# Performance work log

Measured on AMD Instinct MI355X. Metric: run time of the kernel, lower is better.

## Reference

```python
import jax, jax.numpy as jnp
import numpy as np

N, E, T = 10000, 50000, 80000   # nodes, edges, triplets
D, H, C, CF = 16, 128, 64, 64   # n_orb, hidden_dim, conv_dim, coeffs_dim


def l2norm(v):
    # matches torch F.normalize(dim=-1): x / max(||x||_2, 1e-12)
    return v / jnp.maximum(jnp.linalg.norm(v, axis=-1, keepdims=True), 1e-12)


def setup_inputs() -> dict:
    key = jax.random.key(0)
    ks = jax.random.split(key, 16)

    def w(k, i, o):
        return jax.random.normal(k, (i, o), jnp.float32) / np.sqrt(i).astype(np.float32)

    return {
        "x": jax.random.normal(ks[0], (N, H), jnp.float32),
        "cji": jax.random.normal(ks[1], (E, D, CF), jnp.float32),
        "robs": jax.random.normal(ks[2], (E, D), jnp.float32),
        "shbs": jax.random.normal(ks[3], (T, D), jnp.float32),
        "idx_i": jax.random.randint(ks[4], (E,), 0, N),
        "idx_j": jax.random.randint(ks[5], (E,), 0, N),
        "tri_idx_k": jax.random.randint(ks[6], (T,), 0, N),
        "edge_idx_kj": jax.random.randint(ks[7], (T,), 0, E),
        "edge_idx_ji": jax.random.randint(ks[8], (T,), 0, E),
        "W_nb": w(ks[9], H, 2 * C), "b_nb": jnp.zeros((2 * C,), jnp.float32),
        "W_c1": w(ks[10], CF, C),
        "W_c2": w(ks[11], C, 2 * C),
        "W_t3": w(ks[12], C, C), "b_t3": jnp.zeros((C,), jnp.float32),
        "W_n1": w(ks[13], 2 * C, C), "b_n1": jnp.zeros((C,), jnp.float32),
        "W_n2": w(ks[14], C, C), "b_n2": jnp.zeros((C,), jnp.float32),
        "W_na": w(ks[15], C, H),
    }


def reference(x, cji, robs, shbs, idx_i, idx_j, tri_idx_k, edge_idx_kj,
              edge_idx_ji, W_nb, b_nb, W_c1, W_c2, W_t3, b_t3, W_n1, b_n1,
              W_n2, b_n2, W_na):
    silu = jax.nn.silu
    # node_before_lin + chunk
    h = x @ W_nb + b_nb                       # [N, 2C]
    xq, xk = jnp.split(h, 2, axis=-1)         # each [N, C]
    # coeffs_before_lin: act -> Dense -> act -> Dense (no biases)
    c = silu(silu(cji) @ W_c1) @ W_c2         # [E, D, 2C]
    cji2, ckj = jnp.split(c, 2, axis=-1)      # each [E, D, C]
    # triplet gathers
    ckj_g = l2norm(ckj[edge_idx_kj])          # [T, D, C]
    tbo = l2norm(jnp.einsum('td,tdh->th', shbs * robs[edge_idx_kj], ckj_g))  # [T, C]
    tbw = tbo * jax.nn.sigmoid(xk[tri_idx_k])  # [T, C]
    # scatter triplets -> edges (dim_size = robs.size(0) = E)
    agg = jax.ops.segment_sum(tbw, edge_idx_ji, num_segments=E)  # [E, C]
    tbw2 = silu(agg) @ W_t3 + b_t3            # three_lin, [E, C]
    cji3 = l2norm(cji2 * (1.0 + tbw2[:, None, :]))  # cji + cji*w, normalized
    lcao = l2norm(jnp.einsum('ed,edh->eh', robs, cji3))  # [E, C]
    # node message: node_lin on concatenated endpoint features
    m = jnp.concatenate([xq[idx_i], xq[idx_j]], axis=-1)  # [E, 2C]
    m = silu(silu(m) @ W_n1 + b_n1) @ W_n2 + b_n2          # [E, C]
    out = x + jax.ops.segment_sum(lcao * m, idx_i, num_segments=N) @ W_na
    return out
```

## Files before the change

### kernel.cpp

```cpp
#include <hip/hip_runtime.h>
#include <hip/hip_bf16.h>

#define NN 10000
#define EE 50000
#define TT 80000
#define DD 16
#define HH 128
#define CC 64

typedef __hip_bfloat16 bf16;
typedef __attribute__((ext_vector_type(8))) short bf16x8;
typedef __attribute__((ext_vector_type(4))) float f32x4;

__device__ __forceinline__ float silu_f(float x) { return x / (1.f + __expf(-x)); }
__device__ __forceinline__ float sigm_f(float x) { return 1.f / (1.f + __expf(-x)); }

__device__ __forceinline__ short f2bs(float x) {
  __hip_bfloat16 h = __float2bfloat16(x);
  short s;
  __builtin_memcpy(&s, &h, 2);
  return s;
}

__device__ __forceinline__ float rnorm_f(float ss) {
  return __builtin_amdgcn_rcpf(fmaxf(__builtin_amdgcn_sqrtf(ss), 1e-12f));
}

__device__ __forceinline__ float wave_sum64(float v) {
#pragma unroll
  for (int m = 1; m < 64; m <<= 1) v += __shfl_xor(v, m, 64);
  return v;
}

__device__ __forceinline__ void bf2x(unsigned u, float& lo, float& hi) {
  lo = __uint_as_float(u << 16);
  hi = __uint_as_float(u & 0xffff0000u);
}

__global__ __launch_bounds__(128) void k_node(
    const float* __restrict__ x, const float* __restrict__ W_nb,
    const float* __restrict__ b_nb, float* __restrict__ sxq,
    float* __restrict__ sigxk) {
  __shared__ float xrow[HH];
  const int n = blockIdx.x;
  const int t = threadIdx.x;
  xrow[t] = x[(size_t)n * HH + t];
  __syncthreads();
  float acc = b_nb[t];
#pragma unroll 8
  for (int k = 0; k < HH; ++k) acc = fmaf(xrow[k], W_nb[k * HH + t], acc);
  if (t < CC)
    sxq[(size_t)n * CC + t] = silu_f(acc);
  else
    sigxk[(size_t)n * CC + (t - CC)] = sigm_f(acc);
}

#define K2_BLOCKS 2048
#define K2_TILES 50000
__global__ __launch_bounds__(256, 2) void k_coeffs(
    const float* __restrict__ cji, const float* __restrict__ W_c1,
    const float* __restrict__ W_c2, bf16* __restrict__ cji2,
    bf16* __restrict__ ckjn) {
  __shared__ __align__(16) short xbuf[4][16 * 72];
  const int tid = threadIdx.x;
  const int w = tid >> 6, l = tid & 63;
  const int lr = l & 15, lg = l >> 4;
  short* mybuf = xbuf[w];

  bf16x8 b1[2][4];
  bf16x8 b2[2][8];
#pragma unroll
  for (int kt = 0; kt < 2; ++kt) {
#pragma unroll
    for (int nt = 0; nt < 4; ++nt) {
      bf16x8 t;
#pragma unroll
      for (int b = 0; b < 8; ++b)
        t[b] = f2bs(W_c1[(kt * 32 + lg * 8 + b) * 64 + nt * 16 + lr]);
      b1[kt][nt] = t;
    }
#pragma unroll
    for (int nt = 0; nt < 8; ++nt) {
      bf16x8 t;
#pragma unroll
      for (int b = 0; b < 8; ++b)
        t[b] = f2bs(W_c2[(kt * 32 + lg * 8 + b) * 128 + nt * 16 + lr]);
      b2[kt][nt] = t;
    }
  }

  const int nwave = K2_BLOCKS * 4;
  int tile = blockIdx.x * 4 + w;
  if (tile >= K2_TILES) return;

  float4 r0, r1, r2, r3;
  {
    const float* Ab = cji + (size_t)tile * 16 * 64 + lr * 64 + lg * 8;
    r0 = *(const float4*)(Ab);
    r1 = *(const float4*)(Ab + 4);
    r2 = *(const float4*)(Ab + 32);
    r3 = *(const float4*)(Ab + 36);
  }

  for (; tile < K2_TILES; tile += nwave) {
    bf16x8 a0, a1;
    a0[0] = f2bs(silu_f(r0.x)); a0[1] = f2bs(silu_f(r0.y));
    a0[2] = f2bs(silu_f(r0.z)); a0[3] = f2bs(silu_f(r0.w));
    a0[4] = f2bs(silu_f(r1.x)); a0[5] = f2bs(silu_f(r1.y));
    a0[6] = f2bs(silu_f(r1.z)); a0[7] = f2bs(silu_f(r1.w));
    a1[0] = f2bs(silu_f(r2.x)); a1[1] = f2bs(silu_f(r2.y));
    a1[2] = f2bs(silu_f(r2.z)); a1[3] = f2bs(silu_f(r2.w));
    a1[4] = f2bs(silu_f(r3.x)); a1[5] = f2bs(silu_f(r3.y));
    a1[6] = f2bs(silu_f(r3.z)); a1[7] = f2bs(silu_f(r3.w));

    const int next = tile + nwave;
    if (next < K2_TILES) {
      const float* Ab = cji + (size_t)next * 16 * 64 + lr * 64 + lg * 8;
      r0 = *(const float4*)(Ab);
      r1 = *(const float4*)(Ab + 4);
      r2 = *(const float4*)(Ab + 32);
      r3 = *(const float4*)(Ab + 36);
    }

    f32x4 acc1[4];
#pragma unroll
    for (int nt = 0; nt < 4; ++nt) acc1[nt] = (f32x4){0.f, 0.f, 0.f, 0.f};
#pragma unroll
    for (int nt = 0; nt < 4; ++nt) {
      acc1[nt] = __builtin_amdgcn_mfma_f32_16x16x32_bf16(a0, b1[0][nt], acc1[nt], 0, 0, 0);
      acc1[nt] = __builtin_amdgcn_mfma_f32_16x16x32_bf16(a1, b1[1][nt], acc1[nt], 0, 0, 0);
    }

#pragma unroll
    for (int nt = 0; nt < 4; ++nt)
#pragma unroll
      for (int j = 0; j < 4; ++j)
        mybuf[(lg * 4 + j) * 72 + nt * 16 + lr] = f2bs(silu_f(acc1[nt][j]));

    bf16x8 a20 = *(const bf16x8*)(mybuf + lr * 72 + lg * 8);
    bf16x8 a21 = *(const bf16x8*)(mybuf + lr * 72 + 32 + lg * 8);

    f32x4 acc2[8];
#pragma unroll
    for (int nt = 0; nt < 8; ++nt) acc2[nt] = (f32x4){0.f, 0.f, 0.f, 0.f};
#pragma unroll
    for (int nt = 0; nt < 8; ++nt) {
      acc2[nt] = __builtin_amdgcn_mfma_f32_16x16x32_bf16(a20, b2[0][nt], acc2[nt], 0, 0, 0);
      acc2[nt] = __builtin_amdgcn_mfma_f32_16x16x32_bf16(a21, b2[1][nt], acc2[nt], 0, 0, 0);
    }

    float rn[4];
#pragma unroll
    for (int j = 0; j < 4; ++j) {
      float ss = acc2[4][j] * acc2[4][j];
      ss = fmaf(acc2[5][j], acc2[5][j], ss);
      ss = fmaf(acc2[6][j], acc2[6][j], ss);
      ss = fmaf(acc2[7][j], acc2[7][j], ss);
#pragma unroll
      for (int m = 1; m < 16; m <<= 1) ss += __shfl_xor(ss, m, 64);
      rn[j] = rnorm_f(ss);
    }

    union { short h[16]; uint4 u[2]; } p;
#pragma unroll
    for (int nt = 0; nt < 4; ++nt)
#pragma unroll
      for (int j = 0; j < 4; ++j) p.h[nt * 4 + j] = f2bs(acc2[nt][j]);
    {
      uint4* d0 = (uint4*)(cji2 + (size_t)tile * 1024 + l * 16);
      d0[0] = p.u[0];
      d0[1] = p.u[1];
    }
#pragma unroll
    for (int nt = 0; nt < 4; ++nt)
#pragma unroll
      for (int j = 0; j < 4; ++j) p.h[nt * 4 + j] = f2bs(acc2[4 + nt][j] * rn[j]);
    {
      uint4* d1 = (uint4*)(ckjn + (size_t)tile * 1024 + l * 16);
      d1[0] = p.u[0];
      d1[1] = p.u[1];
    }
  }
}

__global__ __launch_bounds__(256) void k_triplet(
    const bf16* __restrict__ ckjn, const float* __restrict__ shbs,
    const float* __restrict__ robs, const float* __restrict__ sigxk,
    const int* __restrict__ tri_idx_k, const int* __restrict__ edge_idx_kj,
    const int* __restrict__ edge_idx_ji, float* __restrict__ agg) {
  const int wid = (blockIdx.x * 256 + threadIdx.x) >> 6;
  const int l = threadIdx.x & 63;
  if (wid >= TT) return;
  const int lq = l >> 4, lr = l & 15;
  const int kj = edge_idx_kj[wid];
  const int kn = tri_idx_k[wid];
  const int ji = edge_idx_ji[wid];
  const float4 sh = *(const float4*)(shbs + (size_t)wid * DD + lq * 4);
  const float4 rb = *(const float4*)(robs + (size_t)kj * DD + lq * 4);
  const float w0 = sh.x * rb.x, w1 = sh.y * rb.y, w2 = sh.z * rb.z,
              w3 = sh.w * rb.w;
  const uint4* base = (const uint4*)(ckjn + (size_t)kj * 1024 + l * 16);
  const uint4 u0 = base[0], u1 = base[1];
  float acc[4];
  {
    float x0, x1, x2, x3;
    bf2x(u0.x, x0, x1); bf2x(u0.y, x2, x3);
    acc[0] = fmaf(w3, x3, fmaf(w2, x2, fmaf(w1, x1, w0 * x0)));
    bf2x(u0.z, x0, x1); bf2x(u0.w, x2, x3);
    acc[1] = fmaf(w3, x3, fmaf(w2, x2, fmaf(w1, x1, w0 * x0)));
    bf2x(u1.x, x0, x1); bf2x(u1.y, x2, x3);
    acc[2] = fmaf(w3, x3, fmaf(w2, x2, fmaf(w1, x1, w0 * x0)));
    bf2x(u1.z, x0, x1); bf2x(u1.w, x2, x3);
    acc[3] = fmaf(w3, x3, fmaf(w2, x2, fmaf(w1, x1, w0 * x0)));
  }
#pragma unroll
  for (int m = 16; m < 64; m <<= 1)
#pragma unroll
    for (int q = 0; q < 4; ++q) acc[q] += __shfl_xor(acc[q], m, 64);
  const float sel = (lq == 0) ? acc[0] : (lq == 1) ? acc[1] : (lq == 2) ? acc[2] : acc[3];
  const float ss = wave_sum64(sel * sel);
  const float tbw = sel * rnorm_f(ss) * sigxk[(size_t)kn * CC + l];
  atomicAdd(&agg[(size_t)ji * CC + l], tbw);
}

#define K4A_TILES 3125
__global__ __launch_bounds__(256, 2) void k_edge_a(
    const float* __restrict__ agg, const float* __restrict__ sxq,
    const int* __restrict__ idx_i, const int* __restrict__ idx_j,
    const float* __restrict__ W_t3, const float* __restrict__ b_t3,
    const float* __restrict__ W_n1, const float* __restrict__ b_n1,
    const float* __restrict__ W_n2, const float* __restrict__ b_n2,
    float* __restrict__ onew_buf, float* __restrict__ m_buf) {
  __shared__ __align__(16) float fbuf[4][16 * 68];
  __shared__ __align__(16) short sbuf[4][16 * 72];
  const int tid = threadIdx.x;
  const int w = tid >> 6, l = tid & 63;
  const int lr = l & 15, lg = l >> 4;
  float* fb = fbuf[w];
  short* sb = sbuf[w];
  const int tile = blockIdx.x * 4 + w;
  if (tile >= K4A_TILES) return;

  bf16x8 bt3[2][4], bn1[4][4], bn2[2][4];
#pragma unroll
  for (int kt = 0; kt < 2; ++kt)
#pragma unroll
    for (int nt = 0; nt < 4; ++nt) {
      bf16x8 t;
#pragma unroll
      for (int b = 0; b < 8; ++b)
        t[b] = f2bs(W_t3[(kt * 32 + lg * 8 + b) * 64 + nt * 16 + lr]);
      bt3[kt][nt] = t;
    }
#pragma unroll
  for (int kt = 0; kt < 4; ++kt)
#pragma unroll
    for (int nt = 0; nt < 4; ++nt) {
      bf16x8 t;
#pragma unroll
      for (int b = 0; b < 8; ++b)
        t[b] = f2bs(W_n1[(kt * 32 + lg * 8 + b) * 64 + nt * 16 + lr]);
      bn1[kt][nt] = t;
    }
#pragma unroll
  for (int kt = 0; kt < 2; ++kt)
#pragma unroll
    for (int nt = 0; nt < 4; ++nt) {
      bf16x8 t;
#pragma unroll
      for (int b = 0; b < 8; ++b)
        t[b] = f2bs(W_n2[(kt * 32 + lg * 8 + b) * 64 + nt * 16 + lr]);
      bn2[kt][nt] = t;
    }
  float bt3c[4], bn1c[4], bn2c[4];
#pragma unroll
  for (int nt = 0; nt < 4; ++nt) {
    bt3c[nt] = b_t3[nt * 16 + lr];
    bn1c[nt] = b_n1[nt * 16 + lr];
    bn2c[nt] = b_n2[nt * 16 + lr];
  }

  const int e = tile * 16 + lr;
  const int vi = idx_i[e], vj = idx_j[e];

  bf16x8 aagg[2];
#pragma unroll
  for (int kt = 0; kt < 2; ++kt) {
    const float4 u = *(const float4*)(agg + (size_t)e * 64 + kt * 32 + lg * 8);
    const float4 v = *(const float4*)(agg + (size_t)e * 64 + kt * 32 + lg * 8 + 4);
    bf16x8 t;
    t[0] = f2bs(silu_f(u.x)); t[1] = f2bs(silu_f(u.y));
    t[2] = f2bs(silu_f(u.z)); t[3] = f2bs(silu_f(u.w));
    t[4] = f2bs(silu_f(v.x)); t[5] = f2bs(silu_f(v.y));
    t[6] = f2bs(silu_f(v.z)); t[7] = f2bs(silu_f(v.w));
    aagg[kt] = t;
  }
  f32x4 acc[4];
#pragma unroll
  for (int nt = 0; nt < 4; ++nt) acc[nt] = (f32x4){0.f, 0.f, 0.f, 0.f};
#pragma unroll
  for (int nt = 0; nt < 4; ++nt) {
    acc[nt] = __builtin_amdgcn_mfma_f32_16x16x32_bf16(aagg[0], bt3[0][nt], acc[nt], 0, 0, 0);
    acc[nt] = __builtin_amdgcn_mfma_f32_16x16x32_bf16(aagg[1], bt3[1][nt], acc[nt], 0, 0, 0);
  }
#pragma unroll
  for (int nt = 0; nt < 4; ++nt)
#pragma unroll
    for (int j = 0; j < 4; ++j)
      fb[(lg * 4 + j) * 68 + nt * 16 + lr] = 1.f + bt3c[nt] + acc[nt][j];
  {
    const int row = l >> 2, cs = (l & 3) * 16;
    float* dst = onew_buf + (size_t)(tile * 16 + row) * 64 + cs;
#pragma unroll
    for (int q = 0; q < 4; ++q)
      *(float4*)(dst + q * 4) = *(const float4*)(fb + row * 68 + cs + q * 4);
  }

  bf16x8 am[4];
#pragma unroll
  for (int kt = 0; kt < 4; ++kt) {
    const float* src = (kt < 2) ? (sxq + (size_t)vi * 64 + kt * 32)
                                : (sxq + (size_t)vj * 64 + (kt - 2) * 32);
    const float4 u = *(const float4*)(src + lg * 8);
    const float4 v = *(const float4*)(src + lg * 8 + 4);
    bf16x8 t;
    t[0] = f2bs(u.x); t[1] = f2bs(u.y); t[2] = f2bs(u.z); t[3] = f2bs(u.w);
    t[4] = f2bs(v.x); t[5] = f2bs(v.y); t[6] = f2bs(v.z); t[7] = f2bs(v.w);
    am[kt] = t;
  }
  f32x4 acc1[4];
#pragma unroll
  for (int nt = 0; nt < 4; ++nt) acc1[nt] = (f32x4){0.f, 0.f, 0.f, 0.f};
#pragma unroll
  for (int nt = 0; nt < 4; ++nt)
#pragma unroll
    for (int kt = 0; kt < 4; ++kt)
      acc1[nt] = __builtin_amdgcn_mfma_f32_16x16x32_bf16(am[kt], bn1[kt][nt], acc1[nt], 0, 0, 0);

#pragma unroll
  for (int nt = 0; nt < 4; ++nt)
#pragma unroll
    for (int j = 0; j < 4; ++j)
      sb[(lg * 4 + j) * 72 + nt * 16 + lr] = f2bs(silu_f(acc1[nt][j] + bn1c[nt]));
  const bf16x8 a20 = *(const bf16x8*)(sb + lr * 72 + lg * 8);
  const bf16x8 a21 = *(const bf16x8*)(sb + lr * 72 + 32 + lg * 8);

  f32x4 acc2[4];
#pragma unroll
  for (int nt = 0; nt < 4; ++nt) acc2[nt] = (f32x4){0.f, 0.f, 0.f, 0.f};
#pragma unroll
  for (int nt = 0; nt < 4; ++nt) {
    acc2[nt] = __builtin_amdgcn_mfma_f32_16x16x32_bf16(a20, bn2[0][nt], acc2[nt], 0, 0, 0);
    acc2[nt] = __builtin_amdgcn_mfma_f32_16x16x32_bf16(a21, bn2[1][nt], acc2[nt], 0, 0, 0);
  }
#pragma unroll
  for (int nt = 0; nt < 4; ++nt)
#pragma unroll
    for (int j = 0; j < 4; ++j)
      fb[(lg * 4 + j) * 68 + nt * 16 + lr] = acc2[nt][j] + bn2c[nt];
  {
    const int row = l >> 2, cs = (l & 3) * 16;
    float* dst = m_buf + (size_t)(tile * 16 + row) * 64 + cs;
#pragma unroll
    for (int q = 0; q < 4; ++q)
      *(float4*)(dst + q * 4) = *(const float4*)(fb + row * 68 + cs + q * 4);
  }
}

__global__ __launch_bounds__(256) void k_edge_b(
    const bf16* __restrict__ cji2, const float* __restrict__ robs,
    const float* __restrict__ onew_buf, const float* __restrict__ m_buf,
    const int* __restrict__ idx_i, float* __restrict__ lacc) {
  const int wid = (blockIdx.x * 256 + threadIdx.x) >> 6;
  const int l = threadIdx.x & 63;
  if (wid >= EE) return;
  const int lq = l >> 4, lr = l & 15;
  const uint4* base = (const uint4*)(cji2 + (size_t)wid * 1024 + l * 16);
  const uint4 u0 = base[0], u1 = base[1];
  const float* ob = onew_buf + (size_t)wid * 64 + lr;
  const float ow0 = ob[0], ow1 = ob[16], ow2 = ob[32], ow3 = ob[48];
  float v[16];
  bf2x(u0.x, v[0], v[1]);  bf2x(u0.y, v[2], v[3]);
  bf2x(u0.z, v[4], v[5]);  bf2x(u0.w, v[6], v[7]);
  bf2x(u1.x, v[8], v[9]);  bf2x(u1.y, v[10], v[11]);
  bf2x(u1.z, v[12], v[13]); bf2x(u1.w, v[14], v[15]);
#pragma unroll
  for (int j = 0; j < 4; ++j) {
    v[j] *= ow0; v[4 + j] *= ow1; v[8 + j] *= ow2; v[12 + j] *= ow3;
  }
  float sq[4];
#pragma unroll
  for (int j = 0; j < 4; ++j)
    sq[j] = fmaf(v[j], v[j],
            fmaf(v[4 + j], v[4 + j],
            fmaf(v[8 + j], v[8 + j], v[12 + j] * v[12 + j])));
#pragma unroll
  for (int m = 1; m < 16; m <<= 1)
#pragma unroll
    for (int j = 0; j < 4; ++j) sq[j] += __shfl_xor(sq[j], m, 64);
  const float4 rb = *(const float4*)(robs + (size_t)wid * DD + lq * 4);
  const float t0 = rb.x * rnorm_f(sq[0]), t1 = rb.y * rnorm_f(sq[1]),
              t2 = rb.z * rnorm_f(sq[2]), t3 = rb.w * rnorm_f(sq[3]);
  float lcq[4];
#pragma unroll
  for (int q = 0; q < 4; ++q)
    lcq[q] = fmaf(t0, v[q * 4 + 0],
             fmaf(t1, v[q * 4 + 1],
             fmaf(t2, v[q * 4 + 2], t3 * v[q * 4 + 3])));
#pragma unroll
  for (int m = 16; m < 64; m <<= 1)
#pragma unroll
    for (int q = 0; q < 4; ++q) lcq[q] += __shfl_xor(lcq[q], m, 64);
  const float sel = (lq == 0) ? lcq[0] : (lq == 1) ? lcq[1] : (lq == 2) ? lcq[2] : lcq[3];
  const float ss = wave_sum64(sel * sel);
  const float lcao = sel * rnorm_f(ss);
  atomicAdd(&lacc[(size_t)idx_i[wid] * CC + l],
            lcao * m_buf[(size_t)wid * 64 + l]);
}

__global__ __launch_bounds__(128) void k_out(
    const float* __restrict__ x, const float* __restrict__ lacc,
    const float* __restrict__ W_na, float* __restrict__ out) {
  __shared__ float lrow[CC];
  const int n = blockIdx.x;
  const int t = threadIdx.x;
  if (t < CC) lrow[t] = lacc[(size_t)n * CC + t];
  __syncthreads();
  float acc = x[(size_t)n * HH + t];
#pragma unroll 8
  for (int k = 0; k < CC; ++k) acc = fmaf(lrow[k], W_na[k * HH + t], acc);
  out[(size_t)n * HH + t] = acc;
}

extern "C" void kernel_launch(void* const* d_in, const int* in_sizes, int n_in,
                              void* d_out, int out_size, void* d_ws,
                              size_t ws_size, hipStream_t stream) {
  const float* x = (const float*)d_in[0];
  const float* cji = (const float*)d_in[1];
  const float* robs = (const float*)d_in[2];
  const float* shbs = (const float*)d_in[3];
  const int* idx_i = (const int*)d_in[4];
  const int* idx_j = (const int*)d_in[5];
  const int* tri_idx_k = (const int*)d_in[6];
  const int* edge_idx_kj = (const int*)d_in[7];
  const int* edge_idx_ji = (const int*)d_in[8];
  const float* W_nb = (const float*)d_in[9];
  const float* b_nb = (const float*)d_in[10];
  const float* W_c1 = (const float*)d_in[11];
  const float* W_c2 = (const float*)d_in[12];
  const float* W_t3 = (const float*)d_in[13];
  const float* b_t3 = (const float*)d_in[14];
  const float* W_n1 = (const float*)d_in[15];
  const float* b_n1 = (const float*)d_in[16];
  const float* W_n2 = (const float*)d_in[17];
  const float* b_n2 = (const float*)d_in[18];
  const float* W_na = (const float*)d_in[19];
  float* out = (float*)d_out;

  char* ws = (char*)d_ws;
  const size_t NC4 = (size_t)NN * CC * 4;
  const size_t EDC2 = (size_t)EE * DD * CC * 2;
  const size_t EC4 = (size_t)EE * CC * 4;
  float* sxq = (float*)(ws);
  float* sigxk = (float*)(ws + NC4);
  bf16* cji2 = (bf16*)(ws + 2 * NC4);
  bf16* ckjn = (bf16*)(ws + 2 * NC4 + EDC2);
  float* agg = (float*)(ws + 2 * NC4 + 2 * EDC2);
  float* lacc = (float*)(ws + 2 * NC4 + 2 * EDC2 + EC4);
  float* onew_buf = (float*)(ws + 2 * NC4 + EDC2);
  float* m_buf = (float*)(ws + 2 * NC4 + EDC2 + EC4);

  hipMemsetAsync(agg, 0, EC4 + NC4, stream);

  k_node<<<NN, 128, 0, stream>>>(x, W_nb, b_nb, sxq, sigxk);
  k_coeffs<<<K2_BLOCKS, 256, 0, stream>>>(cji, W_c1, W_c2, cji2, ckjn);
  k_triplet<<<(TT + 3) / 4, 256, 0, stream>>>(ckjn, shbs, robs, sigxk,
                                              tri_idx_k, edge_idx_kj,
                                              edge_idx_ji, agg);
  k_edge_a<<<(K4A_TILES + 3) / 4, 256, 0, stream>>>(
      agg, sxq, idx_i, idx_j, W_t3, b_t3, W_n1, b_n1, W_n2, b_n2, onew_buf,
      m_buf);
  k_edge_b<<<EE / 4, 256, 0, stream>>>(cji2, robs, onew_buf, m_buf, idx_i,
                                       lacc);
  k_out<<<NN, 128, 0, stream>>>(x, lacc, W_na, out);
}
```

Measured before the change: 232.2 us.

## Process two tiles per wave in coeffs kernel and persist edge_a blocks

New measurement: 252.7 us. +8.8%, slower.

```diff
diff --git a/kernel.cpp b/kernel.cpp
--- a/kernel.cpp
+++ b/kernel.cpp
@@ -55,17 +55,18 @@
     sigxk[(size_t)n * CC + (t - CC)] = sigm_f(acc);
 }
 
-#define K2_BLOCKS 2048
+#define K2_BLOCKS 1024
 #define K2_TILES 50000
 __global__ __launch_bounds__(256, 2) void k_coeffs(
     const float* __restrict__ cji, const float* __restrict__ W_c1,
     const float* __restrict__ W_c2, bf16* __restrict__ cji2,
     bf16* __restrict__ ckjn) {
-  __shared__ __align__(16) short xbuf[4][16 * 72];
+  __shared__ __align__(16) short xbuf[4][2][16 * 72];
   const int tid = threadIdx.x;
   const int w = tid >> 6, l = tid & 63;
   const int lr = l & 15, lg = l >> 4;
-  short* mybuf = xbuf[w];
+  short* buf0 = xbuf[w][0];
+  short* buf1 = xbuf[w][1];
 
   bf16x8 b1[2][4];
   bf16x8 b2[2][8];
@@ -89,96 +90,136 @@
     }
   }
 
-  const int nwave = K2_BLOCKS * 4;
-  int tile = blockIdx.x * 4 + w;
-  if (tile >= K2_TILES) return;
-
-  float4 r0, r1, r2, r3;
-  {
-    const float* Ab = cji + (size_t)tile * 16 * 64 + lr * 64 + lg * 8;
-    r0 = *(const float4*)(Ab);
-    r1 = *(const float4*)(Ab + 4);
-    r2 = *(const float4*)(Ab + 32);
-    r3 = *(const float4*)(Ab + 36);
-  }
-
-  for (; tile < K2_TILES; tile += nwave) {
-    bf16x8 a0, a1;
-    a0[0] = f2bs(silu_f(r0.x)); a0[1] = f2bs(silu_f(r0.y));
-    a0[2] = f2bs(silu_f(r0.z)); a0[3] = f2bs(silu_f(r0.w));
-    a0[4] = f2bs(silu_f(r1.x)); a0[5] = f2bs(silu_f(r1.y));
-    a0[6] = f2bs(silu_f(r1.z)); a0[7] = f2bs(silu_f(r1.w));
-    a1[0] = f2bs(silu_f(r2.x)); a1[1] = f2bs(silu_f(r2.y));
-    a1[2] = f2bs(silu_f(r2.z)); a1[3] = f2bs(silu_f(r2.w));
-    a1[4] = f2bs(silu_f(r3.x)); a1[5] = f2bs(silu_f(r3.y));
-    a1[6] = f2bs(silu_f(r3.z)); a1[7] = f2bs(silu_f(r3.w));
-
-    const int next = tile + nwave;
-    if (next < K2_TILES) {
-      const float* Ab = cji + (size_t)next * 16 * 64 + lr * 64 + lg * 8;
-      r0 = *(const float4*)(Ab);
-      r1 = *(const float4*)(Ab + 4);
-      r2 = *(const float4*)(Ab + 32);
-      r3 = *(const float4*)(Ab + 36);
-    }
-
-    f32x4 acc1[4];
-#pragma unroll
-    for (int nt = 0; nt < 4; ++nt) acc1[nt] = (f32x4){0.f, 0.f, 0.f, 0.f};
-#pragma unroll
-    for (int nt = 0; nt < 4; ++nt) {
-      acc1[nt] = __builtin_amdgcn_mfma_f32_16x16x32_bf16(a0, b1[0][nt], acc1[nt], 0, 0, 0);
-      acc1[nt] = __builtin_amdgcn_mfma_f32_16x16x32_bf16(a1, b1[1][nt], acc1[nt], 0, 0, 0);
+  for (int t0 = blockIdx.x * 8 + w * 2; t0 < K2_TILES; t0 += K2_BLOCKS * 8) {
+    const int t1i = t0 + 1;
+    const float* A0 = cji + (size_t)t0 * 1024 + lr * 64 + lg * 8;
+    const float4 p00 = *(const float4*)(A0);
+    const float4 p01 = *(const float4*)(A0 + 4);
+    const float4 p02 = *(const float4*)(A0 + 32);
+    const float4 p03 = *(const float4*)(A0 + 36);
+    const float* A1 = cji + (size_t)t1i * 1024 + lr * 64 + lg * 8;
+    const float4 p10 = *(const float4*)(A1);
+    const float4 p11 = *(const float4*)(A1 + 4);
+    const float4 p12 = *(const float4*)(A1 + 32);
+    const float4 p13 = *(const float4*)(A1 + 36);
+
+    bf16x8 a00, a01, a10, a11;
+    a00[0] = f2bs(silu_f(p00.x)); a00[1] = f2bs(silu_f(p00.y));
+    a00[2] = f2bs(silu_f(p00.z)); a00[3] = f2bs(silu_f(p00.w));
+    a00[4] = f2bs(silu_f(p01.x)); a00[5] = f2bs(silu_f(p01.y));
+    a00[6] = f2bs(silu_f(p01.z)); a00[7] = f2bs(silu_f(p01.w));
+    a01[0] = f2bs(silu_f(p02.x)); a01[1] = f2bs(silu_f(p02.y));
+    a01[2] = f2bs(silu_f(p02.z)); a01[3] = f2bs(silu_f(p02.w));
+    a01[4] = f2bs(silu_f(p03.x)); a01[5] = f2bs(silu_f(p03.y));
+    a01[6] = f2bs(silu_f(p03.z)); a01[7] = f2bs(silu_f(p03.w));
+    a10[0] = f2bs(silu_f(p10.x)); a10[1] = f2bs(silu_f(p10.y));
+    a10[2] = f2bs(silu_f(p10.z)); a10[3] = f2bs(silu_f(p10.w));
+    a10[4] = f2bs(silu_f(p11.x)); a10[5] = f2bs(silu_f(p11.y));
+    a10[6] = f2bs(silu_f(p11.z)); a10[7] = f2bs(silu_f(p11.w));
+    a11[0] = f2bs(silu_f(p12.x)); a11[1] = f2bs(silu_f(p12.y));
+    a11[2] = f2bs(silu_f(p12.z)); a11[3] = f2bs(silu_f(p12.w));
+    a11[4] = f2bs(silu_f(p13.x)); a11[5] = f2bs(silu_f(p13.y));
+    a11[6] = f2bs(silu_f(p13.z)); a11[7] = f2bs(silu_f(p13.w));
+
+    f32x4 c1a[4], c1b[4];
+#pragma unroll
+    for (int nt = 0; nt < 4; ++nt) {
+      c1a[nt] = (f32x4){0.f, 0.f, 0.f, 0.f};
+      c1b[nt] = (f32x4){0.f, 0.f, 0.f, 0.f};
+    }
+#pragma unroll
+    for (int nt = 0; nt < 4; ++nt) {
+      c1a[nt] = __builtin_amdgcn_mfma_f32_16x16x32_bf16(a00, b1[0][nt], c1a[nt], 0, 0, 0);
+      c1b[nt] = __builtin_amdgcn_mfma_f32_16x16x32_bf16(a10, b1[0][nt], c1b[nt], 0, 0, 0);
+      c1a[nt] = __builtin_amdgcn_mfma_f32_16x16x32_bf16(a01, b1[1][nt], c1a[nt], 0, 0, 0);
+      c1b[nt] = __builtin_amdgcn_mfma_f32_16x16x32_bf16(a11, b1[1][nt], c1b[nt], 0, 0, 0);
     }
 
 #pragma unroll
     for (int nt = 0; nt < 4; ++nt)
 #pragma unroll
-      for (int j = 0; j < 4; ++j)
-        mybuf[(lg * 4 + j) * 72 + nt * 16 + lr] = f2bs(silu_f(acc1[nt][j]));
-
-    bf16x8 a20 = *(const bf16x8*)(mybuf + lr * 72 + lg * 8);
-    bf16x8 a21 = *(const bf16x8*)(mybuf + lr * 72 + 32 + lg * 8);
-
-    f32x4 acc2[8];
-#pragma unroll
-    for (int nt = 0; nt < 8; ++nt) acc2[nt] = (f32x4){0.f, 0.f, 0.f, 0.f};
-#pragma unroll
-    for (int nt = 0; nt < 8; ++nt) {
-      acc2[nt] = __builtin_amdgcn_mfma_f32_16x16x32_bf16(a20, b2[0][nt], acc2[nt], 0, 0, 0);
-      acc2[nt] = __builtin_amdgcn_mfma_f32_16x16x32_bf16(a21, b2[1][nt], acc2[nt], 0, 0, 0);
-    }
-
-    float rn[4];
-#pragma unroll
-    for (int j = 0; j < 4; ++j) {
-      float ss = acc2[4][j] * acc2[4][j];
-      ss = fmaf(acc2[5][j], acc2[5][j], ss);
-      ss = fmaf(acc2[6][j], acc2[6][j], ss);
-      ss = fmaf(acc2[7][j], acc2[7][j], ss);
-#pragma unroll
-      for (int m = 1; m < 16; m <<= 1) ss += __shfl_xor(ss, m, 64);
-      rn[j] = rnorm_f(ss);
-    }
-
-    union { short h[16]; uint4 u[2]; } p;
-#pragma unroll
-    for (int nt = 0; nt < 4; ++nt)
-#pragma unroll
-      for (int j = 0; j < 4; ++j) p.h[nt * 4 + j] = f2bs(acc2[nt][j]);
+      for (int j = 0; j < 4; ++j) {
+        buf0[(lg * 4 + j) * 72 + nt * 16 + lr] = f2bs(silu_f(c1a[nt][j]));
+        buf1[(lg * 4 + j) * 72 + nt * 16 + lr] = f2bs(silu_f(c1b[nt][j]));
+      }
+    const bf16x8 t0a = *(const bf16x8*)(buf0 + lr * 72 + lg * 8);
+    const bf16x8 t0b = *(const bf16x8*)(buf0 + lr * 72 + 32 + lg * 8);
+    const bf16x8 t1a = *(const bf16x8*)(buf1 + lr * 72 + lg * 8);
+    const bf16x8 t1b = *(const bf16x8*)(buf1 + lr * 72 + 32 + lg * 8);
+
     {
-      uint4* d0 = (uint4*)(cji2 + (size_t)tile * 1024 + l * 16);
-      d0[0] = p.u[0];
-      d0[1] = p.u[1];
-    }
-#pragma unroll
-    for (int nt = 0; nt < 4; ++nt)
-#pragma unroll
-      for (int j = 0; j < 4; ++j) p.h[nt * 4 + j] = f2bs(acc2[4 + nt][j] * rn[j]);
+      f32x4 c2a[4], c2b[4];
+#pragma unroll
+      for (int nt = 0; nt < 4; ++nt) {
+        c2a[nt] = (f32x4){0.f, 0.f, 0.f, 0.f};
+        c2b[nt] = (f32x4){0.f, 0.f, 0.f, 0.f};
+      }
+#pragma unroll
+      for (int nt = 0; nt < 4; ++nt) {
+        c2a[nt] = __builtin_amdgcn_mfma_f32_16x16x32_bf16(t0a, b2[0][nt], c2a[nt], 0, 0, 0);
+        c2b[nt] = __builtin_amdgcn_mfma_f32_16x16x32_bf16(t1a, b2[0][nt], c2b[nt], 0, 0, 0);
+        c2a[nt] = __builtin_amdgcn_mfma_f32_16x16x32_bf16(t0b, b2[1][nt], c2a[nt], 0, 0, 0);
+        c2b[nt] = __builtin_amdgcn_mfma_f32_16x16x32_bf16(t1b, b2[1][nt], c2b[nt], 0, 0, 0);
+      }
+      union { short h[16]; uint4 u[2]; } pa, pb;
+#pragma unroll
+      for (int nt = 0; nt < 4; ++nt)
+#pragma unroll
+        for (int j = 0; j < 4; ++j) {
+          pa.h[nt * 4 + j] = f2bs(c2a[nt][j]);
+          pb.h[nt * 4 + j] = f2bs(c2b[nt][j]);
+        }
+      uint4* d0 = (uint4*)(cji2 + (size_t)t0 * 1024 + l * 16);
+      d0[0] = pa.u[0]; d0[1] = pa.u[1];
+      uint4* d1 = (uint4*)(cji2 + (size_t)t1i * 1024 + l * 16);
+      d1[0] = pb.u[0]; d1[1] = pb.u[1];
+    }
+
     {
-      uint4* d1 = (uint4*)(ckjn + (size_t)tile * 1024 + l * 16);
-      d1[0] = p.u[0];
-      d1[1] = p.u[1];
+      f32x4 c3a[4], c3b[4];
+#pragma unroll
+      for (int nt = 0; nt < 4; ++nt) {
+        c3a[nt] = (f32x4){0.f, 0.f, 0.f, 0.f};
+        c3b[nt] = (f32x4){0.f, 0.f, 0.f, 0.f};
+      }
+#pragma unroll
+      for (int nt = 0; nt < 4; ++nt) {
+        c3a[nt] = __builtin_amdgcn_mfma_f32_16x16x32_bf16(t0a, b2[0][4 + nt], c3a[nt], 0, 0, 0);
+        c3b[nt] = __builtin_amdgcn_mfma_f32_16x16x32_bf16(t1a, b2[0][4 + nt], c3b[nt], 0, 0, 0);
+        c3a[nt] = __builtin_amdgcn_mfma_f32_16x16x32_bf16(t0b, b2[1][4 + nt], c3a[nt], 0, 0, 0);
+        c3b[nt] = __builtin_amdgcn_mfma_f32_16x16x32_bf16(t1b, b2[1][4 + nt], c3b[nt], 0, 0, 0);
+      }
+      float rna[4], rnb[4];
+#pragma unroll
+      for (int j = 0; j < 4; ++j) {
+        float sa = c3a[0][j] * c3a[0][j];
+        sa = fmaf(c3a[1][j], c3a[1][j], sa);
+        sa = fmaf(c3a[2][j], c3a[2][j], sa);
+        sa = fmaf(c3a[3][j], c3a[3][j], sa);
+        float sb = c3b[0][j] * c3b[0][j];
+        sb = fmaf(c3b[1][j], c3b[1][j], sb);
+        sb = fmaf(c3b[2][j], c3b[2][j], sb);
+        sb = fmaf(c3b[3][j], c3b[3][j], sb);
+#pragma unroll
+        for (int m = 1; m < 16; m <<= 1) {
+          sa += __shfl_xor(sa, m, 64);
+          sb += __shfl_xor(sb, m, 64);
+        }
+        rna[j] = rnorm_f(sa);
+        rnb[j] = rnorm_f(sb);
+      }
+      union { short h[16]; uint4 u[2]; } pa, pb;
+#pragma unroll
+      for (int nt = 0; nt < 4; ++nt)
+#pragma unroll
+        for (int j = 0; j < 4; ++j) {
+          pa.h[nt * 4 + j] = f2bs(c3a[nt][j] * rna[j]);
+          pb.h[nt * 4 + j] = f2bs(c3b[nt][j] * rnb[j]);
+        }
+      uint4* d0 = (uint4*)(ckjn + (size_t)t0 * 1024 + l * 16);
+      d0[0] = pa.u[0]; d0[1] = pa.u[1];
+      uint4* d1 = (uint4*)(ckjn + (size_t)t1i * 1024 + l * 16);
+      d1[0] = pb.u[0]; d1[1] = pb.u[1];
     }
   }
 }
@@ -224,6 +265,7 @@
 }
 
 #define K4A_TILES 3125
+#define K4A_BLOCKS 256
 __global__ __launch_bounds__(256, 2) void k_edge_a(
     const float* __restrict__ agg, const float* __restrict__ sxq,
     const int* __restrict__ idx_i, const int* __restrict__ idx_j,
@@ -238,8 +280,6 @@
   const int lr = l & 15, lg = l >> 4;
   float* fb = fbuf[w];
   short* sb = sbuf[w];
-  const int tile = blockIdx.x * 4 + w;
-  if (tile >= K4A_TILES) return;
 
   bf16x8 bt3[2][4], bn1[4][4], bn2[2][4];
 #pragma unroll
@@ -280,90 +320,92 @@
     bn2c[nt] = b_n2[nt * 16 + lr];
   }
 
-  const int e = tile * 16 + lr;
-  const int vi = idx_i[e], vj = idx_j[e];
-
-  bf16x8 aagg[2];
-#pragma unroll
-  for (int kt = 0; kt < 2; ++kt) {
-    const float4 u = *(const float4*)(agg + (size_t)e * 64 + kt * 32 + lg * 8);
-    const float4 v = *(const float4*)(agg + (size_t)e * 64 + kt * 32 + lg * 8 + 4);
-    bf16x8 t;
-    t[0] = f2bs(silu_f(u.x)); t[1] = f2bs(silu_f(u.y));
-    t[2] = f2bs(silu_f(u.z)); t[3] = f2bs(silu_f(u.w));
-    t[4] = f2bs(silu_f(v.x)); t[5] = f2bs(silu_f(v.y));
-    t[6] = f2bs(silu_f(v.z)); t[7] = f2bs(silu_f(v.w));
-    aagg[kt] = t;
-  }
-  f32x4 acc[4];
-#pragma unroll
-  for (int nt = 0; nt < 4; ++nt) acc[nt] = (f32x4){0.f, 0.f, 0.f, 0.f};
-#pragma unroll
-  for (int nt = 0; nt < 4; ++nt) {
-    acc[nt] = __builtin_amdgcn_mfma_f32_16x16x32_bf16(aagg[0], bt3[0][nt], acc[nt], 0, 0, 0);
-    acc[nt] = __builtin_amdgcn_mfma_f32_16x16x32_bf16(aagg[1], bt3[1][nt], acc[nt], 0, 0, 0);
-  }
-#pragma unroll
-  for (int nt = 0; nt < 4; ++nt)
-#pragma unroll
-    for (int j = 0; j < 4; ++j)
-      fb[(lg * 4 + j) * 68 + nt * 16 + lr] = 1.f + bt3c[nt] + acc[nt][j];
-  {
-    const int row = l >> 2, cs = (l & 3) * 16;
-    float* dst = onew_buf + (size_t)(tile * 16 + row) * 64 + cs;
-#pragma unroll
-    for (int q = 0; q < 4; ++q)
-      *(float4*)(dst + q * 4) = *(const float4*)(fb + row * 68 + cs + q * 4);
-  }
-
-  bf16x8 am[4];
-#pragma unroll
-  for (int kt = 0; kt < 4; ++kt) {
-    const float* src = (kt < 2) ? (sxq + (size_t)vi * 64 + kt * 32)
-                                : (sxq + (size_t)vj * 64 + (kt - 2) * 32);
-    const float4 u = *(const float4*)(src + lg * 8);
-    const float4 v = *(const float4*)(src + lg * 8 + 4);
-    bf16x8 t;
-    t[0] = f2bs(u.x); t[1] = f2bs(u.y); t[2] = f2bs(u.z); t[3] = f2bs(u.w);
-    t[4] = f2bs(v.x); t[5] = f2bs(v.y); t[6] = f2bs(v.z); t[7] = f2bs(v.w);
-    am[kt] = t;
-  }
-  f32x4 acc1[4];
-#pragma unroll
-  for (int nt = 0; nt < 4; ++nt) acc1[nt] = (f32x4){0.f, 0.f, 0.f, 0.f};
-#pragma unroll
-  for (int nt = 0; nt < 4; ++nt)
-#pragma unroll
-    for (int kt = 0; kt < 4; ++kt)
-      acc1[nt] = __builtin_amdgcn_mfma_f32_16x16x32_bf16(am[kt], bn1[kt][nt], acc1[nt], 0, 0, 0);
-
-#pragma unroll
-  for (int nt = 0; nt < 4; ++nt)
-#pragma unroll
-    for (int j = 0; j < 4; ++j)
-      sb[(lg * 4 + j) * 72 + nt * 16 + lr] = f2bs(silu_f(acc1[nt][j] + bn1c[nt]));
-  const bf16x8 a20 = *(const bf16x8*)(sb + lr * 72 + lg * 8);
-  const bf16x8 a21 = *(const bf16x8*)(sb + lr * 72 + 32 + lg * 8);
-
-  f32x4 acc2[4];
-#pragma unroll
-  for (int nt = 0; nt < 4; ++nt) acc2[nt] = (f32x4){0.f, 0.f, 0.f, 0.f};
-#pragma unroll
-  for (int nt = 0; nt < 4; ++nt) {
-    acc2[nt] = __builtin_amdgcn_mfma_f32_16x16x32_bf16(a20, bn2[0][nt], acc2[nt], 0, 0, 0);
-    acc2[nt] = __builtin_amdgcn_mfma_f32_16x16x32_bf16(a21, bn2[1][nt], acc2[nt], 0, 0, 0);
-  }
-#pragma unroll
-  for (int nt = 0; nt < 4; ++nt)
-#pragma unroll
-    for (int j = 0; j < 4; ++j)
-      fb[(lg * 4 + j) * 68 + nt * 16 + lr] = acc2[nt][j] + bn2c[nt];
-  {
-    const int row = l >> 2, cs = (l & 3) * 16;
-    float* dst = m_buf + (size_t)(tile * 16 + row) * 64 + cs;
-#pragma unroll
-    for (int q = 0; q < 4; ++q)
-      *(float4*)(dst + q * 4) = *(const float4*)(fb + row * 68 + cs + q * 4);
+  for (int tile = blockIdx.x * 4 + w; tile < K4A_TILES; tile += K4A_BLOCKS * 4) {
+    const int e = tile * 16 + lr;
+    const int vi = idx_i[e], vj = idx_j[e];
+
+    bf16x8 aagg[2];
+#pragma unroll
+    for (int kt = 0; kt < 2; ++kt) {
+      const float4 u = *(const float4*)(agg + (size_t)e * 64 + kt * 32 + lg * 8);
+      const float4 v = *(const float4*)(agg + (size_t)e * 64 + kt * 32 + lg * 8 + 4);
+      bf16x8 t;
+      t[0] = f2bs(silu_f(u.x)); t[1] = f2bs(silu_f(u.y));
+      t[2] = f2bs(silu_f(u.z)); t[3] = f2bs(silu_f(u.w));
+      t[4] = f2bs(silu_f(v.x)); t[5] = f2bs(silu_f(v.y));
+      t[6] = f2bs(silu_f(v.z)); t[7] = f2bs(silu_f(v.w));
+      aagg[kt] = t;
+    }
+    f32x4 acc[4];
+#pragma unroll
+    for (int nt = 0; nt < 4; ++nt) acc[nt] = (f32x4){0.f, 0.f, 0.f, 0.f};
+#pragma unroll
+    for (int nt = 0; nt < 4; ++nt) {
+      acc[nt] = __builtin_amdgcn_mfma_f32_16x16x32_bf16(aagg[0], bt3[0][nt], acc[nt], 0, 0, 0);
+      acc[nt] = __builtin_amdgcn_mfma_f32_16x16x32_bf16(aagg[1], bt3[1][nt], acc[nt], 0, 0, 0);
+    }
+#pragma unroll
+    for (int nt = 0; nt < 4; ++nt)
+#pragma unroll
+      for (int j = 0; j < 4; ++j)
+        fb[(lg * 4 + j) * 68 + nt * 16 + lr] = 1.f + bt3c[nt] + acc[nt][j];
+    {
+      const int row = l >> 2, cs = (l & 3) * 16;
+      float* dst = onew_buf + (size_t)(tile * 16 + row) * 64 + cs;
+#pragma unroll
+      for (int q = 0; q < 4; ++q)
+        *(float4*)(dst + q * 4) = *(const float4*)(fb + row * 68 + cs + q * 4);
+    }
+
+    bf16x8 am[4];
+#pragma unroll
+    for (int kt = 0; kt < 4; ++kt) {
+      const float* src = (kt < 2) ? (sxq + (size_t)vi * 64 + kt * 32)
+                                  : (sxq + (size_t)vj * 64 + (kt - 2) * 32);
+      const float4 u = *(const float4*)(src + lg * 8);
+      const float4 v = *(const float4*)(src + lg * 8 + 4);
+      bf16x8 t;
+      t[0] = f2bs(u.x); t[1] = f2bs(u.y); t[2] = f2bs(u.z); t[3] = f2bs(u.w);
+      t[4] = f2bs(v.x); t[5] = f2bs(v.y); t[6] = f2bs(v.z); t[7] = f2bs(v.w);
+      am[kt] = t;
+    }
+    f32x4 acc1[4];
+#pragma unroll
+    for (int nt = 0; nt < 4; ++nt) acc1[nt] = (f32x4){0.f, 0.f, 0.f, 0.f};
+#pragma unroll
+    for (int nt = 0; nt < 4; ++nt)
+#pragma unroll
+      for (int kt = 0; kt < 4; ++kt)
+        acc1[nt] = __builtin_amdgcn_mfma_f32_16x16x32_bf16(am[kt], bn1[kt][nt], acc1[nt], 0, 0, 0);
+
+#pragma unroll
+    for (int nt = 0; nt < 4; ++nt)
+#pragma unroll
+      for (int j = 0; j < 4; ++j)
+        sb[(lg * 4 + j) * 72 + nt * 16 + lr] = f2bs(silu_f(acc1[nt][j] + bn1c[nt]));
+    const bf16x8 a20 = *(const bf16x8*)(sb + lr * 72 + lg * 8);
+    const bf16x8 a21 = *(const bf16x8*)(sb + lr * 72 + 32 + lg * 8);
+
+    f32x4 acc2[4];
+#pragma unroll
+    for (int nt = 0; nt < 4; ++nt) acc2[nt] = (f32x4){0.f, 0.f, 0.f, 0.f};
+#pragma unroll
+    for (int nt = 0; nt < 4; ++nt) {
+      acc2[nt] = __builtin_amdgcn_mfma_f32_16x16x32_bf16(a20, bn2[0][nt], acc2[nt], 0, 0, 0);
+      acc2[nt] = __builtin_amdgcn_mfma_f32_16x16x32_bf16(a21, bn2[1][nt], acc2[nt], 0, 0, 0);
+    }
+#pragma unroll
+    for (int nt = 0; nt < 4; ++nt)
+#pragma unroll
+      for (int j = 0; j < 4; ++j)
+        fb[(lg * 4 + j) * 68 + nt * 16 + lr] = acc2[nt][j] + bn2c[nt];
+    {
+      const int row = l >> 2, cs = (l & 3) * 16;
+      float* dst = m_buf + (size_t)(tile * 16 + row) * 64 + cs;
+#pragma unroll
+      for (int q = 0; q < 4; ++q)
+        *(float4*)(dst + q * 4) = *(const float4*)(fb + row * 68 + cs + q * 4);
+    }
   }
 }
 
@@ -477,7 +519,7 @@
   k_triplet<<<(TT + 3) / 4, 256, 0, stream>>>(ckjn, shbs, robs, sigxk,
                                               tri_idx_k, edge_idx_kj,
                                               edge_idx_ji, agg);
-  k_edge_a<<<(K4A_TILES + 3) / 4, 256, 0, stream>>>(
+  k_edge_a<<<K4A_BLOCKS, 256, 0, stream>>>(
       agg, sxq, idx_i, idx_j, W_t3, b_t3, W_n1, b_n1, W_n2, b_n2, onew_buf,
       m_buf);
   k_edge_b<<<EE / 4, 256, 0, stream>>>(cji2, robs, onew_buf, m_buf, idx_i,
```
